# Kernel optimization log

Hardware: AMD Instinct MI355X
Metric: run time of the kernel (lower is better)

Reference implementation:

```python
import jax, jax.numpy as jnp
import numpy as np

B, S, D, H = 2, 2048, 2048, 32
HD = D // H  # head_dim = 64
ROPE_BASE = 10000.0


def setup_inputs() -> dict:
    key = jax.random.key(0)
    ks = jax.random.split(key, 5)
    x = jax.random.normal(ks[0], (B, S, D), jnp.float32)
    wq = jax.random.normal(ks[1], (D, D), jnp.float32) * 0.02
    wk = jax.random.normal(ks[2], (D, D), jnp.float32) * 0.02
    wv = jax.random.normal(ks[3], (D, D), jnp.float32) * 0.02
    wo = jax.random.normal(ks[4], (D, D), jnp.float32) * 0.02
    # RoPE frequencies, same as llama precompute_freqs_cis: (S, HD//2)
    inv_freq = 1.0 / (ROPE_BASE ** (jnp.arange(0, HD, 2, dtype=jnp.float32) / HD))
    freqs = jnp.outer(jnp.arange(S, dtype=jnp.float32), inv_freq)
    freqs_cos = jnp.cos(freqs)
    freqs_sin = jnp.sin(freqs)
    # additive causal mask (1,1,S,S): 0 on/below diagonal, -1e9 above
    mask = jnp.where(jnp.tril(jnp.ones((S, S), bool)), 0.0, -1e9).astype(jnp.float32)[None, None]
    return {"x": x, "wq": wq, "wk": wk, "wv": wv, "wo": wo,
            "freqs_cos": freqs_cos, "freqs_sin": freqs_sin, "mask": mask}


def _rope(t, cos, sin):
    # t: [b, s, h, d]; cos/sin: [s, d//2]; interleaved complex rotation
    tr, ti = t[..., 0::2], t[..., 1::2]
    c = cos[None, :, None, :]
    s = sin[None, :, None, :]
    out_r = tr * c - ti * s
    out_i = tr * s + ti * c
    return jnp.stack([out_r, out_i], axis=-1).reshape(t.shape)


def reference(x, wq, wk, wv, wo, freqs_cos, freqs_sin, mask):
    b, s, _ = x.shape
    q = (x @ wq).reshape(b, s, H, HD)
    k = (x @ wk).reshape(b, s, H, HD)
    v = (x @ wv).reshape(b, s, H, HD)
    q = _rope(q, freqs_cos, freqs_sin)
    k = _rope(k, freqs_cos, freqs_sin)
    # [b, h, s, d]
    q = q.transpose(0, 2, 1, 3)
    k = k.transpose(0, 2, 1, 3)
    v = v.transpose(0, 2, 1, 3)
    scores = jnp.einsum('bhqd,bhkd->bhqk', q, k) / np.sqrt(HD).astype(np.float32)
    scores = scores + mask
    probs = jax.nn.softmax(scores.astype(jnp.float32), axis=-1).astype(q.dtype)
    out = jnp.einsum('bhqk,bhkd->bhqd', probs, v)
    out = out.transpose(0, 2, 1, 3).reshape(b, s, H * HD)
    return out @ wo
```

## Files before the change

### kernel.cpp

```cpp
#include <hip/hip_runtime.h>
#include <hip/hip_bf16.h>
#include <stdint.h>

typedef unsigned short u16;
typedef __attribute__((ext_vector_type(4))) float f32x4;
typedef __attribute__((ext_vector_type(8))) short s16x8;
typedef __attribute__((ext_vector_type(4))) short s16x4;

#define B_  2
#define S_  2048
#define D_  2048
#define H_  32
#define HD_ 64

static __device__ __forceinline__ float bf2f(u16 u) {
    union { uint32_t i; float f; } v; v.i = ((uint32_t)u) << 16; return v.f;
}
static __device__ __forceinline__ u16 f2bf(float f) {
    union { float f; uint32_t i; } v; v.f = f;
    uint32_t r = v.i + 0x7FFFu + ((v.i >> 16) & 1u);
    return (u16)(r >> 16);
}
static __device__ __forceinline__ bool probe_f32(const u16* fc) {
    return *(const uint32_t*)fc == 0x3F800000u;
}
static __device__ __forceinline__ void gload_lds16(const void* g, void* l) {
    __builtin_amdgcn_global_load_lds(
        (const __attribute__((address_space(1))) uint32_t*)g,
        (__attribute__((address_space(3))) uint32_t*)l, 16, 0, 0);
}

__global__ __launch_bounds__(256) void k_cast_x(const void* __restrict__ in,
    const u16* __restrict__ fc, u16* __restrict__ out)
{
    const bool f32 = probe_f32(fc);
    const size_t i = ((size_t)blockIdx.x * 256 + threadIdx.x) * 8;
    if (f32) {
        const float* inf = (const float*)in;
        f32x4 lo = *(const f32x4*)(inf + i);
        f32x4 hi = *(const f32x4*)(inf + i + 4);
        s16x8 o;
        #pragma unroll
        for (int j = 0; j < 4; ++j) {
            o[j]     = (short)f2bf(lo[j]);
            o[4 + j] = (short)f2bf(hi[j]);
        }
        *(s16x8*)(out + i) = o;
    } else {
        *(s16x8*)(out + i) = *(const s16x8*)((const u16*)in + i);
    }
}

#define G3_NT 64

static __device__ __forceinline__ void gemm_pipe_body(
    const u16* __restrict__ A, const u16* __restrict__ Bt,
    void* __restrict__ Cv, const int c_f32, const int N,
    u16 (*__restrict__ AB)[12288])
{
    const int tid = threadIdx.x;
    const int lane = tid & 63;
    const int w = tid >> 6;
    const int wr = w >> 2, wc = w & 3;
    const int l15 = lane & 15, l4 = lane >> 4;
    const int brow = blockIdx.y * 256, bcol = blockIdx.x * 128;
    const int K = 2048;

    f32x4 acc[8][2];
    #pragma unroll
    for (int m = 0; m < 8; ++m)
        #pragma unroll
        for (int n = 0; n < 2; ++n)
            acc[m][n] = (f32x4){0.f, 0.f, 0.f, 0.f};

    auto STAGE = [&](int b, int t) {
        u16* buf = AB[b];
        const int kt = t * 32;
        #pragma unroll
        for (int i = 0; i < 2; ++i) {
            const int ca = i * 512 + tid;
            const int row = ca >> 2, cc = ca & 3;
            const int ccs = cc ^ (row & 3);
            gload_lds16(A + (size_t)(brow + row) * K + kt + ccs * 8,
                        buf + (size_t)(i * 512 + (tid & ~63)) * 8);
        }
        const int cb = tid;
        const int rowb = cb >> 2, ccb = (cb & 3) ^ (rowb & 3);
        gload_lds16(Bt + (size_t)(bcol + rowb) * K + kt + ccb * 8,
                    buf + 8192 + (size_t)(tid & ~63) * 8);
    };

    auto COMPUTE = [&](int b) {
        const u16* Ad = AB[b];
        const u16* Bd = AB[b] + 8192;
        s16x8 af[8], bf[2];
        #pragma unroll
        for (int m = 0; m < 8; ++m) {
            const int row = wr * 128 + m * 16 + l15;
            af[m] = *(const s16x8*)(Ad + row * 32 + ((l4 ^ (row & 3)) << 3));
        }
        #pragma unroll
        for (int n = 0; n < 2; ++n) {
            const int row = wc * 32 + n * 16 + l15;
            bf[n] = *(const s16x8*)(Bd + row * 32 + ((l4 ^ (row & 3)) << 3));
        }
        #pragma unroll
        for (int m = 0; m < 8; ++m)
            #pragma unroll
            for (int n = 0; n < 2; ++n)
                acc[m][n] = __builtin_amdgcn_mfma_f32_16x16x32_bf16(af[m], bf[n], acc[m][n], 0, 0, 0);
    };

    STAGE(0, 0);
    STAGE(1, 1);
    STAGE(2, 2);
    for (int t = 0; t < G3_NT; ++t) {
        if (t < G3_NT - 2)       asm volatile("s_waitcnt vmcnt(6)" ::: "memory");
        else if (t == G3_NT - 2) asm volatile("s_waitcnt vmcnt(3)" ::: "memory");
        else                     asm volatile("s_waitcnt vmcnt(0)" ::: "memory");
        __builtin_amdgcn_s_barrier();
        if (t + 3 < G3_NT) STAGE((t + 3) & 3, t + 3);
        COMPUTE(t & 3);
    }

    #pragma unroll
    for (int m = 0; m < 8; ++m) {
        const int row = brow + wr * 128 + m * 16 + l4 * 4;
        #pragma unroll
        for (int n = 0; n < 2; ++n) {
            const int col = bcol + wc * 32 + n * 16 + l15;
            #pragma unroll
            for (int r = 0; r < 4; ++r) {
                if (c_f32)
                    ((float*)Cv)[(size_t)(row + r) * N + col] = acc[m][n][r];
                else
                    ((u16*)Cv)[(size_t)(row + r) * N + col] = f2bf(acc[m][n][r]);
            }
        }
    }
}

__global__ __launch_bounds__(512, 2) void k_gemm_qkv(const u16* __restrict__ xb,
    const u16* __restrict__ wqt, const u16* __restrict__ wkt, const u16* __restrict__ wvt,
    u16* __restrict__ Q, u16* __restrict__ Kc, u16* __restrict__ V)
{
    __shared__ u16 AB[4][12288];
    const u16* Bt = (blockIdx.z == 0) ? wqt : (blockIdx.z == 1) ? wkt : wvt;
    u16* C = (blockIdx.z == 0) ? Q : (blockIdx.z == 1) ? Kc : V;
    gemm_pipe_body(xb, Bt, C, 0, D_, AB);
}

__global__ __launch_bounds__(512, 2) void k_gemm_out(const u16* __restrict__ A,
    const u16* __restrict__ Bt, const u16* __restrict__ fc, void* __restrict__ C)
{
    __shared__ u16 AB[4][12288];
    const int f32 = probe_f32(fc) ? 1 : 0;
    gemm_pipe_body(A, Bt, C, f32, D_, AB);
}

__global__ __launch_bounds__(256) void k_prep_w(const void* __restrict__ in,
    const u16* __restrict__ fc, u16* __restrict__ out)
{
    __shared__ u16 t[64][72];
    const bool f32 = probe_f32(fc);
    const int tid = threadIdx.x;
    const int r0 = blockIdx.y * 64, c0 = blockIdx.x * 64;
    #pragma unroll
    for (int i = 0; i < 2; ++i) {
        const int chunk = i * 256 + tid;
        const int row = chunk >> 3, cc = chunk & 7;
        if (f32) {
            const float* inf = (const float*)in;
            const size_t off = (size_t)(r0 + row) * 2048 + c0 + cc * 8;
            f32x4 lo = *(const f32x4*)(inf + off);
            f32x4 hi = *(const f32x4*)(inf + off + 4);
            #pragma unroll
            for (int j = 0; j < 4; ++j) {
                t[row][cc * 8 + j]     = f2bf(lo[j]);
                t[row][cc * 8 + 4 + j] = f2bf(hi[j]);
            }
        } else {
            s16x8 v = *(const s16x8*)((const u16*)in + (size_t)(r0 + row) * 2048 + c0 + cc * 8);
            *(s16x8*)&t[row][cc * 8] = v;
        }
    }
    __syncthreads();
    #pragma unroll
    for (int i = 0; i < 2; ++i) {
        const int chunk = i * 256 + tid;
        const int orow = chunk >> 3, occ = chunk & 7;
        s16x8 v;
        #pragma unroll
        for (int j = 0; j < 8; ++j) v[j] = (short)t[occ * 8 + j][orow];
        *(s16x8*)(out + (size_t)(c0 + orow) * 2048 + r0 + occ * 8) = v;
    }
}

__global__ __launch_bounds__(256) void k_rope_layout(const u16* __restrict__ Q,
    const u16* __restrict__ K, const u16* __restrict__ V,
    const u16* __restrict__ fc, const u16* __restrict__ fs,
    u16* __restrict__ Qr, u16* __restrict__ Kr, u16* __restrict__ Vt)
{
    __shared__ u16 vt[64][72];
    const bool f32 = probe_f32(fc);
    const float QS = 0.125f * 1.4426950408889634f;
    const int tid = threadIdx.x;
    const int s0 = blockIdx.x * 64;
    const int head = blockIdx.y;
    const int b = head >> 5, h = head & 31;
    const size_t hb = (size_t)head * S_ * HD_;
    #pragma unroll
    for (int i = 0; i < 2; ++i) {
        const int chunk = i * 256 + tid;
        const int sr = chunk >> 3, cc = chunk & 7;
        const int s = s0 + sr;
        const size_t src = ((size_t)(b * S_ + s)) * D_ + h * HD_ + cc * 8;
        float c[4], sn[4];
        if (f32) {
            const float* fcf = (const float*)fc;
            const float* fsf = (const float*)fs;
            #pragma unroll
            for (int j = 0; j < 4; ++j) {
                c[j]  = fcf[s * 32 + cc * 4 + j];
                sn[j] = fsf[s * 32 + cc * 4 + j];
            }
        } else {
            #pragma unroll
            for (int j = 0; j < 4; ++j) {
                c[j]  = bf2f(fc[s * 32 + cc * 4 + j]);
                sn[j] = bf2f(fs[s * 32 + cc * 4 + j]);
            }
        }
        s16x8 vq = *(const s16x8*)(Q + src);
        s16x8 vk = *(const s16x8*)(K + src);
        s16x8 oq, ok;
        #pragma unroll
        for (int j = 0; j < 4; ++j) {
            float qr = bf2f((u16)vq[2 * j]), qi = bf2f((u16)vq[2 * j + 1]);
            oq[2 * j]     = (short)f2bf((qr * c[j] - qi * sn[j]) * QS);
            oq[2 * j + 1] = (short)f2bf((qr * sn[j] + qi * c[j]) * QS);
            float kr = bf2f((u16)vk[2 * j]), ki = bf2f((u16)vk[2 * j + 1]);
            ok[2 * j]     = (short)f2bf(kr * c[j] - ki * sn[j]);
            ok[2 * j + 1] = (short)f2bf(kr * sn[j] + ki * c[j]);
        }
        *(s16x8*)(Qr + hb + (size_t)s * HD_ + cc * 8) = oq;
        *(s16x8*)(Kr + hb + (size_t)s * HD_ + cc * 8) = ok;
        s16x8 vv = *(const s16x8*)(V + src);
        *(s16x8*)&vt[sr][cc * 8] = vv;
    }
    __syncthreads();
    #pragma unroll
    for (int i = 0; i < 2; ++i) {
        const int chunk = i * 256 + tid;
        const int hd = chunk >> 3, sc = chunk & 7;
        s16x8 v;
        #pragma unroll
        for (int j = 0; j < 8; ++j) v[j] = (short)vt[sc * 8 + j][hd];
        *(s16x8*)(Vt + hb + (size_t)hd * S_ + s0 + sc * 8) = v;
    }
}

__global__ __launch_bounds__(512, 2) void k_flash(const u16* __restrict__ Qr,
    const u16* __restrict__ Kr, const u16* __restrict__ Vt, u16* __restrict__ O)
{
    __shared__ u16 Ks[2][64][64];
    __shared__ u16 Vs[2][64][64];
    __shared__ u16 p_lds[8][32][72];
    const int tid = threadIdx.x;
    const int lane = tid & 63, w = tid >> 6;
    const int l15 = lane & 15, l4 = lane >> 4;
    const int bxp = blockIdx.x;
    const int stripe = (w < 4) ? bxp : (15 - bxp);
    const int head = blockIdx.y;
    const int b = head >> 5, h = head & 31;
    const size_t hb = (size_t)head * S_ * HD_;
    const u16* Qh = Qr + hb;
    const u16* Kh = Kr + hb;
    const u16* Vh = Vt + hb;
    const int q0 = stripe * 128 + (w & 3) * 32;
    const int td = stripe * 2 + ((w & 3) >> 1);
    const int T  = 2 * (15 - bxp) + 2;

    s16x8 aq[2][2];
    #pragma unroll
    for (int m = 0; m < 2; ++m) {
        aq[m][0] = *(const s16x8*)(Qh + (size_t)(q0 + m * 16 + l15) * 64 + 0  + l4 * 8);
        aq[m][1] = *(const s16x8*)(Qh + (size_t)(q0 + m * 16 + l15) * 64 + 32 + l4 * 8);
    }
    s16x8 vone;
    #pragma unroll
    for (int j = 0; j < 8; ++j) vone[j] = (short)0x3F80;

    f32x4 oac[2][4];
    f32x4 osum[2];
    #pragma unroll
    for (int m = 0; m < 2; ++m) {
        osum[m] = (f32x4){0.f, 0.f, 0.f, 0.f};
        #pragma unroll
        for (int n = 0; n < 4; ++n) oac[m][n] = (f32x4){0.f, 0.f, 0.f, 0.f};
    }

    const int srow = tid >> 3;
    const int sc8  = tid & 7;

    {
        s16x8 k0 = *(const s16x8*)(Kh + (size_t)srow * 64 + sc8 * 8);
        s16x8 v0 = *(const s16x8*)(Vh + (size_t)srow * S_ + sc8 * 8);
        const int cs = (sc8 ^ (srow & 7)) * 8;
        *(s16x8*)&Ks[0][srow][cs] = k0;
        *(s16x8*)&Vs[0][srow][cs] = v0;
    }

    for (int t = 0; t < T; ++t) {
        const int cb = t & 1;
        __syncthreads();
        s16x8 kn, vn;
        const bool pf = (t + 1 < T);
        if (pf) {
            const int kvn = (t + 1) * 64;
            kn = *(const s16x8*)(Kh + (size_t)(kvn + srow) * 64 + sc8 * 8);
            vn = *(const s16x8*)(Vh + (size_t)srow * S_ + kvn + sc8 * 8);
        }
        if (t <= td) {
            const int kv0 = t * 64;
            const bool masked = (t == td);
            s16x8 bk0[4], bk1[4];
            #pragma unroll
            for (int n = 0; n < 4; ++n) {
                const int row = n * 16 + l15;
                bk0[n] = *(const s16x8*)&Ks[cb][row][((l4      ^ (row & 7)) << 3)];
                bk1[n] = *(const s16x8*)&Ks[cb][row][(((4 + l4) ^ (row & 7)) << 3)];
            }
            f32x4 s4[2][4];
            #pragma unroll
            for (int m = 0; m < 2; ++m)
                #pragma unroll
                for (int n = 0; n < 4; ++n) {
                    f32x4 z = (f32x4){0.f, 0.f, 0.f, 0.f};
                    z = __builtin_amdgcn_mfma_f32_16x16x32_bf16(bk0[n], aq[m][0], z, 0, 0, 0);
                    z = __builtin_amdgcn_mfma_f32_16x16x32_bf16(bk1[n], aq[m][1], z, 0, 0, 0);
                    s4[m][n] = z;
                }
            #pragma unroll
            for (int m = 0; m < 2; ++m)
                #pragma unroll
                for (int n = 0; n < 4; ++n) {
                    s16x4 pk;
                    #pragma unroll
                    for (int r = 0; r < 4; ++r) {
                        float sv = s4[m][n][r];
                        if (masked) {
                            const int kcol = kv0 + n * 16 + l4 * 4 + r;
                            const int qrow = q0 + m * 16 + l15;
                            if (kcol > qrow) sv = -1.0e30f;
                        }
                        pk[r] = (short)f2bf(exp2f(sv));
                    }
                    *(s16x4*)&p_lds[w][m * 16 + l15][n * 16 + l4 * 4] = pk;
                }
            asm volatile("s_waitcnt lgkmcnt(0)" ::: "memory");
            #pragma unroll
            for (int kk = 0; kk < 2; ++kk) {
                s16x8 pa[2];
                #pragma unroll
                for (int m = 0; m < 2; ++m)
                    pa[m] = *(const s16x8*)&p_lds[w][m * 16 + l15][kk * 32 + l4 * 8];
                #pragma unroll
                for (int n = 0; n < 4; ++n) {
                    const int row = n * 16 + l15;
                    s16x8 bv = *(const s16x8*)&Vs[cb][row][(((kk * 4 + l4) ^ (row & 7)) << 3)];
                    #pragma unroll
                    for (int m = 0; m < 2; ++m)
                        oac[m][n] = __builtin_amdgcn_mfma_f32_16x16x32_bf16(pa[m], bv, oac[m][n], 0, 0, 0);
                }
                #pragma unroll
                for (int m = 0; m < 2; ++m)
                    osum[m] = __builtin_amdgcn_mfma_f32_16x16x32_bf16(pa[m], vone, osum[m], 0, 0, 0);
            }
        }
        if (pf) {
            const int nb = cb ^ 1;
            const int cs = (sc8 ^ (srow & 7)) * 8;
            *(s16x8*)&Ks[nb][srow][cs] = kn;
            *(s16x8*)&Vs[nb][srow][cs] = vn;
        }
    }

    #pragma unroll
    for (int m = 0; m < 2; ++m)
        #pragma unroll
        for (int r = 0; r < 4; ++r) {
            const float rl = 1.0f / osum[m][r];
            const int qrow = q0 + m * 16 + l4 * 4 + r;
            #pragma unroll
            for (int n = 0; n < 4; ++n)
                O[(size_t)(b * S_ + qrow) * D_ + h * HD_ + n * 16 + l15] = f2bf(oac[m][n][r] * rl);
        }
}

extern "C" void kernel_launch(void* const* d_in, const int* in_sizes, int n_in,
                              void* d_out, int out_size, void* d_ws, size_t ws_size,
                              hipStream_t stream)
{
    const void* x  = d_in[0];
    const void* wq = d_in[1];
    const void* wk = d_in[2];
    const void* wv = d_in[3];
    const void* wo = d_in[4];
    const u16* fc = (const u16*)d_in[5];
    const u16* fs = (const u16*)d_in[6];

    u16* ws = (u16*)d_ws;
    const size_t WSZ = (size_t)D_ * D_;
    const size_t TSZ = (size_t)B_ * S_ * D_;
    u16* wqt = ws;
    u16* wkt = wqt + WSZ;
    u16* wvt = wkt + WSZ;
    u16* wot = wvt + WSZ;
    u16* Qb  = wot + WSZ;
    u16* Kb  = Qb + TSZ;
    u16* Vb  = Kb + TSZ;
    u16* Qr  = Vb + TSZ;
    u16* Kr  = Qr + TSZ;
    u16* Vt  = Kr + TSZ;
    u16* Ob  = Qb;
    u16* xb  = Qr;

    if (ws_size < (4 * WSZ + 6 * TSZ) * sizeof(u16)) return;

    dim3 blk(256);
    dim3 blk512(512);
    k_cast_x<<<dim3((unsigned)(TSZ / 2048)), blk, 0, stream>>>(x, fc, xb);
    k_prep_w<<<dim3(32, 32), blk, 0, stream>>>(wq, fc, wqt);
    k_prep_w<<<dim3(32, 32), blk, 0, stream>>>(wk, fc, wkt);
    k_prep_w<<<dim3(32, 32), blk, 0, stream>>>(wv, fc, wvt);
    k_prep_w<<<dim3(32, 32), blk, 0, stream>>>(wo, fc, wot);
    k_gemm_qkv<<<dim3(16, 16, 3), blk512, 0, stream>>>(xb, wqt, wkt, wvt, Qb, Kb, Vb);
    k_rope_layout<<<dim3(32, 64), blk, 0, stream>>>(Qb, Kb, Vb, fc, fs, Qr, Kr, Vt);
    k_flash<<<dim3(8, 64), blk512, 0, stream>>>(Qr, Kr, Vt, Ob);
    k_gemm_out<<<dim3(16, 16), blk512, 0, stream>>>(Ob, wot, fc, d_out);
}
```

Baseline: 330.4 us.

## Double GEMM K-tile to 64 with 3-stage pipeline and XCD-aware block swizzle

The projection GEMMs now stage 64-wide K tiles (two MFMA k-steps per barrier) in a 3-buffer ring instead of 32-wide tiles in a 4-buffer ring. This halves the number of barriers and waitcnt points per tile. Block indices are also remapped so that consecutive blocks, which are spread round-robin across the 8 XCDs, share A/B tiles in each XCD's L2. LDS use grows from 96KB to 144KB per block, which may cut the 2-blocks-per-CU occupancy.

```diff
diff --git a/kernel.cpp b/kernel.cpp
--- a/kernel.cpp
+++ b/kernel.cpp
@@ -51,19 +51,19 @@
     }
 }
 
-#define G3_NT 64
+#define G4_NT 32
 
 static __device__ __forceinline__ void gemm_pipe_body(
     const u16* __restrict__ A, const u16* __restrict__ Bt,
     void* __restrict__ Cv, const int c_f32, const int N,
-    u16 (*__restrict__ AB)[12288])
+    const int brow, const int bcol,
+    u16 (*__restrict__ AB)[24576])
 {
     const int tid = threadIdx.x;
     const int lane = tid & 63;
     const int w = tid >> 6;
     const int wr = w >> 2, wc = w & 3;
     const int l15 = lane & 15, l4 = lane >> 4;
-    const int brow = blockIdx.y * 256, bcol = blockIdx.x * 128;
     const int K = 2048;
 
     f32x4 acc[8][2];
@@ -75,52 +75,57 @@
 
     auto STAGE = [&](int b, int t) {
         u16* buf = AB[b];
-        const int kt = t * 32;
-        #pragma unroll
-        for (int i = 0; i < 2; ++i) {
+        const int kt = t * 64;
+        #pragma unroll
+        for (int i = 0; i < 4; ++i) {
             const int ca = i * 512 + tid;
-            const int row = ca >> 2, cc = ca & 3;
-            const int ccs = cc ^ (row & 3);
+            const int row = ca >> 3, cc = ca & 7;
+            const int ccs = cc ^ (row & 7);
             gload_lds16(A + (size_t)(brow + row) * K + kt + ccs * 8,
                         buf + (size_t)(i * 512 + (tid & ~63)) * 8);
         }
-        const int cb = tid;
-        const int rowb = cb >> 2, ccb = (cb & 3) ^ (rowb & 3);
-        gload_lds16(Bt + (size_t)(bcol + rowb) * K + kt + ccb * 8,
-                    buf + 8192 + (size_t)(tid & ~63) * 8);
+        #pragma unroll
+        for (int i = 0; i < 2; ++i) {
+            const int cb = i * 512 + tid;
+            const int row = cb >> 3, cc = cb & 7;
+            const int ccs = cc ^ (row & 7);
+            gload_lds16(Bt + (size_t)(bcol + row) * K + kt + ccs * 8,
+                        buf + 16384 + (size_t)(i * 512 + (tid & ~63)) * 8);
+        }
     };
 
     auto COMPUTE = [&](int b) {
         const u16* Ad = AB[b];
-        const u16* Bd = AB[b] + 8192;
-        s16x8 af[8], bf[2];
-        #pragma unroll
-        for (int m = 0; m < 8; ++m) {
-            const int row = wr * 128 + m * 16 + l15;
-            af[m] = *(const s16x8*)(Ad + row * 32 + ((l4 ^ (row & 3)) << 3));
-        }
-        #pragma unroll
-        for (int n = 0; n < 2; ++n) {
-            const int row = wc * 32 + n * 16 + l15;
-            bf[n] = *(const s16x8*)(Bd + row * 32 + ((l4 ^ (row & 3)) << 3));
-        }
-        #pragma unroll
-        for (int m = 0; m < 8; ++m)
-            #pragma unroll
-            for (int n = 0; n < 2; ++n)
-                acc[m][n] = __builtin_amdgcn_mfma_f32_16x16x32_bf16(af[m], bf[n], acc[m][n], 0, 0, 0);
+        const u16* Bd = AB[b] + 16384;
+        #pragma unroll
+        for (int kk = 0; kk < 2; ++kk) {
+            s16x8 af[8], bf[2];
+            #pragma unroll
+            for (int m = 0; m < 8; ++m) {
+                const int row = wr * 128 + m * 16 + l15;
+                af[m] = *(const s16x8*)(Ad + row * 64 + (((kk * 4 + l4) ^ (row & 7)) << 3));
+            }
+            #pragma unroll
+            for (int n = 0; n < 2; ++n) {
+                const int row = wc * 32 + n * 16 + l15;
+                bf[n] = *(const s16x8*)(Bd + row * 64 + (((kk * 4 + l4) ^ (row & 7)) << 3));
+            }
+            #pragma unroll
+            for (int m = 0; m < 8; ++m)
+                #pragma unroll
+                for (int n = 0; n < 2; ++n)
+                    acc[m][n] = __builtin_amdgcn_mfma_f32_16x16x32_bf16(af[m], bf[n], acc[m][n], 0, 0, 0);
+        }
     };
 
     STAGE(0, 0);
     STAGE(1, 1);
-    STAGE(2, 2);
-    for (int t = 0; t < G3_NT; ++t) {
-        if (t < G3_NT - 2)       asm volatile("s_waitcnt vmcnt(6)" ::: "memory");
-        else if (t == G3_NT - 2) asm volatile("s_waitcnt vmcnt(3)" ::: "memory");
-        else                     asm volatile("s_waitcnt vmcnt(0)" ::: "memory");
+    for (int t = 0; t < G4_NT; ++t) {
+        if (t < G4_NT - 1) asm volatile("s_waitcnt vmcnt(6)" ::: "memory");
+        else               asm volatile("s_waitcnt vmcnt(0)" ::: "memory");
         __builtin_amdgcn_s_barrier();
-        if (t + 3 < G3_NT) STAGE((t + 3) & 3, t + 3);
-        COMPUTE(t & 3);
+        if (t + 2 < G4_NT) STAGE((t + 2) % 3, t + 2);
+        COMPUTE(t % 3);
     }
 
     #pragma unroll
@@ -144,18 +149,24 @@
     const u16* __restrict__ wqt, const u16* __restrict__ wkt, const u16* __restrict__ wvt,
     u16* __restrict__ Q, u16* __restrict__ Kc, u16* __restrict__ V)
 {
-    __shared__ u16 AB[4][12288];
-    const u16* Bt = (blockIdx.z == 0) ? wqt : (blockIdx.z == 1) ? wkt : wvt;
-    u16* C = (blockIdx.z == 0) ? Q : (blockIdx.z == 1) ? Kc : V;
-    gemm_pipe_body(xb, Bt, C, 0, D_, AB);
+    __shared__ u16 AB[3][24576];
+    const int lin = blockIdx.x + 16 * (blockIdx.y + 16 * blockIdx.z);
+    const int swz = (lin & 7) * 96 + (lin >> 3);
+    const int bx = swz & 15, by = (swz >> 4) & 15, bz = swz >> 8;
+    const u16* Bt = (bz == 0) ? wqt : (bz == 1) ? wkt : wvt;
+    u16* C = (bz == 0) ? Q : (bz == 1) ? Kc : V;
+    gemm_pipe_body(xb, Bt, C, 0, D_, by * 256, bx * 128, AB);
 }
 
 __global__ __launch_bounds__(512, 2) void k_gemm_out(const u16* __restrict__ A,
     const u16* __restrict__ Bt, const u16* __restrict__ fc, void* __restrict__ C)
 {
-    __shared__ u16 AB[4][12288];
+    __shared__ u16 AB[3][24576];
     const int f32 = probe_f32(fc) ? 1 : 0;
-    gemm_pipe_body(A, Bt, C, f32, D_, AB);
+    const int lin = blockIdx.x + 16 * blockIdx.y;
+    const int swz = (lin & 7) * 32 + (lin >> 3);
+    const int bx = swz & 15, by = swz >> 4;
+    gemm_pipe_body(A, Bt, C, f32, D_, by * 256, bx * 128, AB);
 }
 
 __global__ __launch_bounds__(256) void k_prep_w(const void* __restrict__ in,
```

New measurement: 305.4 us. 7.6% less time.
